# Performance work log

Hardware: AMD Instinct MI355X
Metric: run time of the kernel (lower is better)

## Reference

```python
import jax, jax.numpy as jnp
import numpy as np

BITS = 3
LEVELS = 2 ** BITS            # 8
HALF_RANGE = (LEVELS - 1) / 2  # 3.5
INCREMENT = 1.0 / (LEVELS // 2)  # 0.25


def setup_inputs() -> dict:
    key = jax.random.key(0)
    kq, kk, kv, kr = jax.random.split(key, 4)
    B, H, S, D = 2, 16, 2048, 128
    q = jax.random.normal(kq, (B, H, S, D), dtype=jnp.float32)
    k = jax.random.normal(kk, (B, H, S, D), dtype=jnp.float32)
    v = jax.random.normal(kv, (B, H, S, D), dtype=jnp.float32)
    # random orthogonal rotation (QR of a Gaussian), as in PolarQuant.__init__
    Hmat = jax.random.normal(kr, (D, D), dtype=jnp.float32)
    R, _ = jnp.linalg.qr(Hmat)
    qjl_scale = jnp.full((1,), 0.01, dtype=jnp.float32)
    return {"q": q, "k": k, "v": v, "R": R, "qjl_scale": qjl_scale}


def _compress_decompress(x, R, qjl_scale):
    """PolarQuant rotate -> QJL 3-bit quantize (+ sign correction) -> dequantize -> inverse rotate."""
    B, Hh, S, D = x.shape
    xr = jnp.einsum('bhsd,de->bhse', x, R)            # rotate: x @ R
    x_max = jnp.abs(xr).max() + 1e-8                   # global scale (as in quantize/compress)
    xs = xr / x_max * HALF_RANGE                       # scale to [-3.5, 3.5]
    xq = jnp.clip(jnp.round(xs / INCREMENT) * INCREMENT, -HALF_RANGE, HALF_RANGE)
    residual = xs - xq
    xc = xq + jnp.sign(residual) * qjl_scale[0] * x_max  # QJL 1-bit correction
    xd = xc / HALF_RANGE * x_max                       # dequantize
    xo = jnp.einsum('bhse,de->bhsd', xd, R)            # inverse rotate: y @ R.T
    return xo


def reference(q, k, v, R, qjl_scale):
    D = q.shape[-1]
    k_approx = _compress_decompress(k, R, qjl_scale)
    v_approx = _compress_decompress(v, R, qjl_scale)
    scores = jnp.einsum('bhqd,bhkd->bhqk', q, k_approx) / jnp.sqrt(jnp.float32(D))
    attn = jax.nn.softmax(scores, axis=-1)
    out = jnp.einsum('bhqk,bhkd->bhqd', attn, v_approx)
    return out
```

## Files before the change

### kernel.cpp

```cpp
#include <hip/hip_runtime.h>


typedef float    f32x4  __attribute__((ext_vector_type(4)));
typedef float    f32x16 __attribute__((ext_vector_type(16)));
typedef __bf16   bf16x8 __attribute__((ext_vector_type(8)));
typedef __bf16   bf16x4 __attribute__((ext_vector_type(4)));
typedef _Float16 f16x8  __attribute__((ext_vector_type(8)));
typedef short    s16x4  __attribute__((ext_vector_type(4)));
typedef unsigned long long u64;

#define SLEN 2048
#define DH   128

static __device__ __forceinline__ f32x16 zero16() {
  f32x16 z;
#pragma unroll
  for (int i = 0; i < 16; ++i) z[i] = 0.f;
  return z;
}

static __device__ __forceinline__ f32x16 mfma_bf16_32x32x16(bf16x8 a, bf16x8 b, f32x16 c) {
  return __builtin_amdgcn_mfma_f32_32x32x16_bf16(a, b, c, 0, 0, 0);
}
static __device__ __forceinline__ f32x16 mfma_f16_32x32x16(f16x8 a, f16x8 b, f32x16 c) {
  return __builtin_amdgcn_mfma_f32_32x32x16_f16(a, b, c, 0, 0, 0);
}
static __device__ __forceinline__ f32x16 mfma_bf16_32x32x8(s16x4 a, s16x4 b, f32x16 c) {
  return __builtin_amdgcn_mfma_f32_32x32x8bf16_1k(a, b, c, 0, 0, 0);
}

static __device__ __forceinline__ void lds_dma16(const void* g, void* l) {
  __builtin_amdgcn_global_load_lds(
      (const __attribute__((address_space(1))) void*)(unsigned long long)g,
      (__attribute__((address_space(3))) void*)(unsigned int)(unsigned long long)l,
      16, 0, 0);
}

static __device__ __forceinline__ float qdq(float xr, float xmax, float qs) {
  float xs = xr / xmax * 3.5f;
  float xq = rintf(xs * 4.0f) * 0.25f;
  xq = fminf(3.5f, fmaxf(-3.5f, xq));
  float res = xs - xq;
  float sg = (res > 0.0f) ? 1.0f : ((res < 0.0f) ? -1.0f : 0.0f);
  float xc = xq + sg * qs * xmax;
  return xc / 3.5f * xmax;
}

static __device__ __forceinline__ unsigned short bfbits(float f) {
  __bf16 b = (__bf16)f;
  return __builtin_bit_cast(unsigned short, b);
}

__global__ __launch_bounds__(256) void prep_R(
    const float* __restrict__ R, _Float16* __restrict__ Bhi,
    _Float16* __restrict__ Blo, _Float16* __restrict__ BhiT,
    _Float16* __restrict__ BloT)
{
  int i = blockIdx.x * 256 + threadIdx.x;
  int kk = i >> 7, n = i & 127;
  float r = R[i];
  _Float16 h = (_Float16)r;
  _Float16 l = (_Float16)(r - (float)h);
  Bhi[i] = h; Blo[i] = l;
  BhiT[n * 128 + kk] = h; BloT[n * 128 + kk] = l;
}

template<int NT, int MODE>
static __device__ __forceinline__ void rot_body(
    const float* __restrict__ X, const _Float16* __restrict__ Gh,
    const _Float16* __restrict__ Gl, void* __restrict__ OUTv,
    float* __restrict__ part, float* __restrict__ qn, int bid)
{
  __shared__ _Float16 BH[128 * 128];
  __shared__ _Float16 BL[(NT == 3) ? 128 * 128 : 8];

  const int tid = threadIdx.x, wave = tid >> 6, lane = tid & 63;
  const int r31 = lane & 31, hi = lane >> 5;
  const long r0 = (long)bid * 128;

#pragma unroll
  for (int u = 0; u < 8; ++u) {
    int c = (wave * 8 + u) * 64 + lane;
    int n = c >> 4, p = c & 15, ch = p ^ (n & 7);
    lds_dma16(Gh + n * 128 + ch * 8, BH + (wave * 8 + u) * 512);
    if constexpr (NT == 3)
      lds_dma16(Gl + n * 128 + ch * 8, BL + (wave * 8 + u) * 512);
  }

  const long rowg = r0 + wave * 32 + r31;
  f16x8 ah[8], al[8];
#pragma unroll
  for (int t = 0; t < 8; ++t) {
    f32x4 x0 = *(const f32x4*)&X[rowg * 128 + t * 16 + hi * 8];
    f32x4 x1 = *(const f32x4*)&X[rowg * 128 + t * 16 + hi * 8 + 4];
#pragma unroll
    for (int j = 0; j < 4; ++j) {
      _Float16 h0 = (_Float16)x0[j]; ah[t][j] = h0;
      _Float16 h1 = (_Float16)x1[j]; ah[t][4 + j] = h1;
      if constexpr (NT == 3) {
        al[t][j]     = (_Float16)(x0[j] - (float)h0);
        al[t][4 + j] = (_Float16)(x1[j] - (float)h1);
      }
    }
  }
  __syncthreads();

  f32x16 acc[4];
#pragma unroll
  for (int ct = 0; ct < 4; ++ct) acc[ct] = zero16();

#pragma unroll
  for (int ct = 0; ct < 4; ++ct) {
#pragma unroll
    for (int t = 0; t < 8; ++t) {
      int idx = (ct * 32 + r31) * 128 + (((2 * t + hi) ^ (r31 & 7)) * 8);
      f16x8 bh = *(const f16x8*)&BH[idx];
      acc[ct] = mfma_f16_32x32x16(ah[t], bh, acc[ct]);
      if constexpr (NT == 3) {
        f16x8 bl = *(const f16x8*)&BL[idx];
        acc[ct] = mfma_f16_32x32x16(ah[t], bl, acc[ct]);
        acc[ct] = mfma_f16_32x32x16(al[t], bh, acc[ct]);
      }
    }
  }

  if constexpr (MODE == 0) {
    float* OUT = (float*)OUTv;
    float am = 0.f;
#pragma unroll
    for (int ct = 0; ct < 4; ++ct)
#pragma unroll
      for (int r = 0; r < 16; ++r) {
        long grow = r0 + wave * 32 + (r & 3) + 8 * (r >> 2) + 4 * hi;
        float v = acc[ct][r];
        OUT[grow * 128 + ct * 32 + r31] = v;
        am = fmaxf(am, fabsf(v));
      }
#pragma unroll
    for (int m = 1; m <= 32; m <<= 1) am = fmaxf(am, __shfl_xor(am, m, 64));
    if (lane == 0) part[bid * 4 + wave] = am;
  } else if constexpr (MODE == 1) {
    __bf16* OUT = (__bf16*)OUTv;
    const float sc = 0.08838834764831843f;
    float rs[16];
#pragma unroll
    for (int r = 0; r < 16; ++r) rs[r] = 0.f;
#pragma unroll
    for (int ct = 0; ct < 4; ++ct)
#pragma unroll
      for (int r = 0; r < 16; ++r) {
        long grow = r0 + wave * 32 + (r & 3) + 8 * (r >> 2) + 4 * hi;
        __bf16 b = (__bf16)(acc[ct][r] * sc);
        OUT[grow * 128 + ct * 32 + r31] = b;
        float fb = (float)b;
        rs[r] += fb * fb;
      }
#pragma unroll
    for (int r = 0; r < 16; ++r) {
#pragma unroll
      for (int msk = 1; msk <= 16; msk <<= 1) rs[r] += __shfl_xor(rs[r], msk, 64);
      if (r31 == r)
        qn[r0 + wave * 32 + (r & 3) + 8 * (r >> 2) + 4 * hi] = sqrtf(rs[r]);
    }
  } else {
    float* OUT = (float*)OUTv;
#pragma unroll
    for (int ct = 0; ct < 4; ++ct)
#pragma unroll
      for (int r = 0; r < 16; ++r) {
        long grow = r0 + wave * 32 + (r & 3) + 8 * (r >> 2) + 4 * hi;
        OUT[grow * 128 + ct * 32 + r31] = acc[ct][r];
      }
  }
}

__global__ __launch_bounds__(256) void rot_kv_kernel(
    const float* __restrict__ K, const float* __restrict__ V,
    const _Float16* __restrict__ Gh, const _Float16* __restrict__ Gl,
    float* __restrict__ kr, float* __restrict__ vr,
    float* __restrict__ kpart, float* __restrict__ vpart)
{
  const bool isv = blockIdx.x >= 512;
  rot_body<3, 0>(isv ? V : K, Gh, Gl, isv ? (void*)vr : (void*)kr,
                 isv ? vpart : kpart, nullptr, blockIdx.x & 511);
}

__global__ __launch_bounds__(256) void rot_q_kernel(
    const float* __restrict__ X, const _Float16* __restrict__ Gh,
    const _Float16* __restrict__ Gl, __bf16* __restrict__ qb,
    float* __restrict__ qn)
{
  rot_body<1, 1>(X, Gh, Gl, (void*)qb, nullptr, qn, blockIdx.x);
}

__global__ __launch_bounds__(256) void rot_o_kernel(
    const float* __restrict__ X, const _Float16* __restrict__ Gh,
    const _Float16* __restrict__ Gl, float* __restrict__ out)
{
  rot_body<1, 2>(X, Gh, Gl, (void*)out, nullptr, nullptr, blockIdx.x);
}

__global__ __launch_bounds__(256) void quantize_vt_kernel(
    const float* __restrict__ vr, const float* __restrict__ vpart,
    const float* __restrict__ qjl, u64* __restrict__ vdt2)
{
  __shared__ unsigned int Ts32[128][18];
  __shared__ float sm[4];
  const int tid = threadIdx.x;

  float m = 0.f;
  for (int i = tid; i < 2048; i += 256) m = fmaxf(m, vpart[i]);
#pragma unroll
  for (int msk = 1; msk <= 32; msk <<= 1) m = fmaxf(m, __shfl_xor(m, msk, 64));
  if ((tid & 63) == 0) sm[tid >> 6] = m;
  __syncthreads();
  const float xmax = fmaxf(fmaxf(sm[0], sm[1]), fmaxf(sm[2], sm[3])) + 1e-8f;
  const float qs = qjl[0];

  const int bh = blockIdx.x >> 6, blk = blockIdx.x & 63;
  const int s0 = blk * 32;
  const int sp  = tid & 15;
  const int dch = tid >> 4;
  const long rb = (long)bh * SLEN + s0;
  const float* p0 = &vr[(rb + sp * 2    ) * 128 + dch * 8];
  const float* p1 = &vr[(rb + sp * 2 + 1) * 128 + dch * 8];
#pragma unroll
  for (int j = 0; j < 8; ++j) {
    unsigned a = bfbits(qdq(p0[j], xmax, qs));
    unsigned b = bfbits(qdq(p1[j], xmax, qs));
    Ts32[dch * 8 + j][sp] = a | (b << 16);
  }
  __syncthreads();
  const long obase = (long)(bh * 64 + blk) * 1024;
#pragma unroll
  for (int u = 0; u < 4; ++u) {
    int idx = u * 256 + tid;
    int g = idx >> 7, d = idx & 127;
    vdt2[obase + idx] = *(const u64*)&Ts32[d][2 * g];
  }
}

__global__ __launch_bounds__(256) void quantize_k_kernel(
    const float* __restrict__ kr, const float* __restrict__ kpart,
    const float* __restrict__ qjl, __bf16* __restrict__ out)
{
  __shared__ float sm[4];
  const int tid = threadIdx.x;
  float m = 0.f;
  for (int i = tid; i < 2048; i += 256) m = fmaxf(m, kpart[i]);
#pragma unroll
  for (int msk = 1; msk <= 32; msk <<= 1) m = fmaxf(m, __shfl_xor(m, msk, 64));
  if ((tid & 63) == 0) sm[tid >> 6] = m;
  __syncthreads();
  const float xmax = fmaxf(fmaxf(sm[0], sm[1]), fmaxf(sm[2], sm[3])) + 1e-8f;
  const float qs = qjl[0];

  long i = ((long)blockIdx.x * 256 + tid) * 4;
  f32x4 x = *(const f32x4*)&kr[i];
  bf16x4 ov;
#pragma unroll
  for (int j = 0; j < 4; ++j) ov[j] = (__bf16)qdq(x[j], xmax, qs);
  *(bf16x4*)&out[i] = ov;
}

__global__ __launch_bounds__(256) void attn2(
    const __bf16* __restrict__ qb, const __bf16* __restrict__ kd,
    const u64* __restrict__ vdt2, const float* __restrict__ qn,
    const float* __restrict__ kpart, const float* __restrict__ qjl,
    float* __restrict__ orot)
{
  __shared__ __attribute__((aligned(16))) __bf16 Ks[2][32 * DH];
  __shared__ __attribute__((aligned(16))) u64   Vt[2][1024];
  __shared__ float Ls[4][32];
  __shared__ float sm[4];

  const int tid = threadIdx.x, wave = tid >> 6, lane = tid & 63;
  const int r31 = lane & 31, hi = lane >> 5;
  const int head = blockIdx.x & 31, qt = blockIdx.x >> 5;
  const long hrow = (long)head * SLEN;
  const int qrow0 = qt * 128 + wave * 32;

  float km = 0.f;
  for (int i = tid; i < 2048; i += 256) km = fmaxf(km, kpart[i]);
#pragma unroll
  for (int m = 1; m <= 32; m <<= 1) km = fmaxf(km, __shfl_xor(km, m, 64));
  if (lane == 0) sm[wave] = km;
  __syncthreads();
  const float xmax = fmaxf(fmaxf(sm[0], sm[1]), fmaxf(sm[2], sm[3])) + 1e-8f;
  const float Bk = 11.313708499f * ((3.5f + qjl[0] * xmax) * xmax / 3.5f) * 1.02f * 0.5f;

  bf16x8 qf[8];
#pragma unroll
  for (int t = 0; t < 8; ++t)
    qf[t] = *(const bf16x8*)&qb[(hrow + qrow0 + r31) * DH + t * 16 + hi * 8];
  const float Mq = qn[hrow + qrow0 + r31] * Bk;

  int koff[8];
#pragma unroll
  for (int t = 0; t < 8; ++t)
    koff[t] = r31 * 256 + (((2 * t + hi) ^ (r31 & 7)) << 4);

  const __bf16* ksrc[2]; int kds[2];
#pragma unroll
  for (int u = 0; u < 2; ++u) {
    int c = (wave * 2 + u) * 64 + lane;
    int row = c >> 4, ch = (c & 15) ^ (row & 7);
    ksrc[u] = kd + (hrow + row) * DH + ch * 8;
    kds[u] = (wave * 2 + u) * 512;
  }
  const char* vbase = (const char*)(vdt2 + (long)head * 64 * 1024);
  const char* vsrc[2];
#pragma unroll
  for (int u = 0; u < 2; ++u)
    vsrc[u] = vbase + (long)((wave * 2 + u) * 64 + lane) * 16;

#pragma unroll
  for (int t0 = 0; t0 < 2; ++t0) {
    lds_dma16(ksrc[0] + (long)t0 * 32 * DH, &Ks[t0][kds[0]]);
    lds_dma16(ksrc[1] + (long)t0 * 32 * DH, &Ks[t0][kds[1]]);
    lds_dma16(vsrc[0] + (long)t0 * 8192, &Vt[t0][(wave * 2 + 0) * 128]);
    lds_dma16(vsrc[1] + (long)t0 * 8192, &Vt[t0][(wave * 2 + 1) * 128]);
  }
  asm volatile("s_waitcnt vmcnt(4)" ::: "memory");
  __builtin_amdgcn_s_barrier();
  asm volatile("" ::: "memory");

  f32x16 acc[4];
#pragma unroll
  for (int dt = 0; dt < 4; ++dt) acc[dt] = zero16();
  float ls0 = 0.f, ls1 = 0.f, ls2 = 0.f, ls3 = 0.f;

#pragma unroll 2
  for (int kt = 0; kt < SLEN / 32; ++kt) {
    const int cur = kt & 1;

    f32x16 s = zero16();
    __builtin_amdgcn_s_setprio(1);
#pragma unroll
    for (int t = 0; t < 8; ++t) {
      bf16x8 ka = *(const bf16x8*)((const char*)&Ks[cur][0] + koff[t]);
      s = mfma_bf16_32x32x16(ka, qf[t], s);
    }
    __builtin_amdgcn_s_setprio(0);

    float p[16];
#pragma unroll
    for (int r = 0; r < 16; ++r) p[r] = __expf(s[r] - Mq);
#pragma unroll
    for (int r = 0; r < 16; r += 4) {
      ls0 += p[r]; ls1 += p[r + 1]; ls2 += p[r + 2]; ls3 += p[r + 3];
    }

    __builtin_amdgcn_s_setprio(1);
#pragma unroll
    for (int st = 0; st < 4; ++st) {
      bf16x4 pb;
#pragma unroll
      for (int j = 0; j < 4; ++j) pb[j] = (__bf16)p[st * 4 + j];
      s16x4 pa = __builtin_bit_cast(s16x4, pb);
#pragma unroll
      for (int dt = 0; dt < 4; ++dt) {
        s16x4 vb = __builtin_bit_cast(s16x4, Vt[cur][(st * 2 + hi) * 128 + dt * 32 + r31]);
        acc[dt] = mfma_bf16_32x32x8(pa, vb, acc[dt]);
      }
    }
    __builtin_amdgcn_s_setprio(0);

    if (kt < SLEN / 32 - 1) {
      asm volatile("s_waitcnt vmcnt(0)" ::: "memory");
      __builtin_amdgcn_s_barrier();
      asm volatile("" ::: "memory");
      if (kt < SLEN / 32 - 2) {
        const long ko = (long)(kt + 2) * 32 * DH;
        const long vo = (long)(kt + 2) * 8192;
        lds_dma16(ksrc[0] + ko, &Ks[cur][kds[0]]);
        lds_dma16(ksrc[1] + ko, &Ks[cur][kds[1]]);
        lds_dma16(vsrc[0] + vo, &Vt[cur][(wave * 2 + 0) * 128]);
        lds_dma16(vsrc[1] + vo, &Vt[cur][(wave * 2 + 1) * 128]);
      }
    }
  }

  float lsum = (ls0 + ls1) + (ls2 + ls3);
  lsum += __shfl_xor(lsum, 32, 64);
  if (hi == 0) Ls[wave][r31] = 1.0f / lsum;
  __syncthreads();

#pragma unroll
  for (int dt = 0; dt < 4; ++dt)
#pragma unroll
    for (int r = 0; r < 16; ++r) {
      int qr = (r & 3) + 8 * (r >> 2) + 4 * hi;
      orot[(hrow + qrow0 + qr) * DH + dt * 32 + r31] = acc[dt][r] * Ls[wave][qr];
    }
}

extern "C" void kernel_launch(void* const* d_in, const int* in_sizes, int n_in,
                              void* d_out, int out_size, void* d_ws, size_t ws_size,
                              hipStream_t stream)
{
  const float* q   = (const float*)d_in[0];
  const float* k   = (const float*)d_in[1];
  const float* v   = (const float*)d_in[2];
  const float* R   = (const float*)d_in[3];
  const float* qjl = (const float*)d_in[4];

  char* ws = (char*)d_ws;
  float* kpart = (float*)ws;
  float* vpart = (float*)(ws + 8192);
  _Float16* Bhi  = (_Float16*)(ws + 32768);
  _Float16* Blo  = (_Float16*)(ws + 65536);
  _Float16* BhiT = (_Float16*)(ws + 98304);
  _Float16* BloT = (_Float16*)(ws + 131072);
  float* qn = (float*)(ws + 163840);
  char* base = ws + 425984;
  __bf16* qb   = (__bf16*)base;
  float*  kr   = (float*)(base + (16u << 20));
  float*  vr   = (float*)(base + (48u << 20));
  u64*    vdt2 = (u64*)(base + (80u << 20));
  __bf16* kd   = (__bf16*)vr;
  float* orot  = kr;

  dim3 b256(256);
  prep_R<<<64, b256, 0, stream>>>(R, Bhi, Blo, BhiT, BloT);
  rot_kv_kernel<<<1024, b256, 0, stream>>>(k, v, BhiT, BloT, kr, vr, kpart, vpart);
  rot_q_kernel<<<512, b256, 0, stream>>>(q, BhiT, BloT, qb, qn);
  quantize_vt_kernel<<<2048, b256, 0, stream>>>(vr, vpart, qjl, vdt2);
  quantize_k_kernel<<<8192, b256, 0, stream>>>(kr, kpart, qjl, kd);
  attn2<<<512, b256, 0, stream>>>(qb, kd, vdt2, qn, kpart, qjl, orot);
  rot_o_kernel<<<512, b256, 0, stream>>>(orot, Bhi, Blo, (float*)d_out);
}
```

Before: 321.3 us.

## Process two key tiles per iteration with 32x32x16 PV MFMAs and exp2 softmax

```diff
diff --git a/kernel.cpp b/kernel.cpp
--- a/kernel.cpp
+++ b/kernel.cpp
@@ -6,7 +6,6 @@
 typedef __bf16   bf16x8 __attribute__((ext_vector_type(8)));
 typedef __bf16   bf16x4 __attribute__((ext_vector_type(4)));
 typedef _Float16 f16x8  __attribute__((ext_vector_type(8)));
-typedef short    s16x4  __attribute__((ext_vector_type(4)));
 typedef unsigned long long u64;
 
 #define SLEN 2048
@@ -24,9 +23,6 @@
 }
 static __device__ __forceinline__ f32x16 mfma_f16_32x32x16(f16x8 a, f16x8 b, f32x16 c) {
   return __builtin_amdgcn_mfma_f32_32x32x16_f16(a, b, c, 0, 0, 0);
-}
-static __device__ __forceinline__ f32x16 mfma_bf16_32x32x8(s16x4 a, s16x4 b, f32x16 c) {
-  return __builtin_amdgcn_mfma_f32_32x32x8bf16_1k(a, b, c, 0, 0, 0);
 }
 
 static __device__ __forceinline__ void lds_dma16(const void* g, void* l) {
@@ -141,7 +137,7 @@
     if (lane == 0) part[bid * 4 + wave] = am;
   } else if constexpr (MODE == 1) {
     __bf16* OUT = (__bf16*)OUTv;
-    const float sc = 0.08838834764831843f;
+    const float sc = 0.12751743342f;
     float rs[16];
 #pragma unroll
     for (int r = 0; r < 16; ++r) rs[r] = 0.f;
@@ -233,10 +229,13 @@
   __syncthreads();
   const long obase = (long)(bh * 64 + blk) * 1024;
 #pragma unroll
-  for (int u = 0; u < 4; ++u) {
-    int idx = u * 256 + tid;
-    int g = idx >> 7, d = idx & 127;
-    vdt2[obase + idx] = *(const u64*)&Ts32[d][2 * g];
+  for (int uu = 0; uu < 2; ++uu) {
+    int u_ = uu * 256 + tid;
+    int half = u_ >> 8, hi = (u_ >> 7) & 1, d = u_ & 127;
+    u64 qlo = *(const u64*)&Ts32[d][2 * (half * 4 + hi)];
+    u64 qhi = *(const u64*)&Ts32[d][2 * (half * 4 + hi + 2)];
+    vdt2[obase + u_ * 2    ] = qlo;
+    vdt2[obase + u_ * 2 + 1] = qhi;
   }
 }
 
@@ -263,14 +262,14 @@
   *(bf16x4*)&out[i] = ov;
 }
 
-__global__ __launch_bounds__(256) void attn2(
+__global__ __launch_bounds__(256, 2) void attn2(
     const __bf16* __restrict__ qb, const __bf16* __restrict__ kd,
     const u64* __restrict__ vdt2, const float* __restrict__ qn,
     const float* __restrict__ kpart, const float* __restrict__ qjl,
     float* __restrict__ orot)
 {
-  __shared__ __attribute__((aligned(16))) __bf16 Ks[2][32 * DH];
-  __shared__ __attribute__((aligned(16))) u64   Vt[2][1024];
+  __shared__ __attribute__((aligned(16))) __bf16 Ks[2][2][32 * DH];
+  __shared__ __attribute__((aligned(16))) u64   Vt[2][2][1024];
   __shared__ float Ls[4][32];
   __shared__ float sm[4];
 
@@ -293,12 +292,19 @@
 #pragma unroll
   for (int t = 0; t < 8; ++t)
     qf[t] = *(const bf16x8*)&qb[(hrow + qrow0 + r31) * DH + t * 16 + hi * 8];
-  const float Mq = qn[hrow + qrow0 + r31] * Bk;
+  const float mqneg = -(qn[hrow + qrow0 + r31] * Bk);
 
   int koff[8];
 #pragma unroll
   for (int t = 0; t < 8; ++t)
     koff[t] = r31 * 256 + (((2 * t + hi) ^ (r31 & 7)) << 4);
+
+  int vof0[4], vof1[4];
+#pragma unroll
+  for (int dt = 0; dt < 4; ++dt) {
+    vof0[dt] = (((0 * 2 + hi) * 128) + dt * 32 + r31) * 16;
+    vof1[dt] = (((1 * 2 + hi) * 128) + dt * 32 + r31) * 16;
+  }
 
   const __bf16* ksrc[2]; int kds[2];
 #pragma unroll
@@ -314,14 +320,22 @@
   for (int u = 0; u < 2; ++u)
     vsrc[u] = vbase + (long)((wave * 2 + u) * 64 + lane) * 16;
 
-#pragma unroll
-  for (int t0 = 0; t0 < 2; ++t0) {
-    lds_dma16(ksrc[0] + (long)t0 * 32 * DH, &Ks[t0][kds[0]]);
-    lds_dma16(ksrc[1] + (long)t0 * 32 * DH, &Ks[t0][kds[1]]);
-    lds_dma16(vsrc[0] + (long)t0 * 8192, &Vt[t0][(wave * 2 + 0) * 128]);
-    lds_dma16(vsrc[1] + (long)t0 * 8192, &Vt[t0][(wave * 2 + 1) * 128]);
-  }
-  asm volatile("s_waitcnt vmcnt(4)" ::: "memory");
+  auto STAGE = [&](int B, int P) {
+    const long k0 = (long)(2 * P) * 32 * DH, k1 = k0 + 32 * DH;
+    const long v0 = (long)(2 * P) * 8192,    v1 = v0 + 8192;
+    lds_dma16(ksrc[0] + k0, &Ks[B][0][kds[0]]);
+    lds_dma16(ksrc[1] + k0, &Ks[B][0][kds[1]]);
+    lds_dma16(ksrc[0] + k1, &Ks[B][1][kds[0]]);
+    lds_dma16(ksrc[1] + k1, &Ks[B][1][kds[1]]);
+    lds_dma16(vsrc[0] + v0, &Vt[B][0][(wave * 2 + 0) * 128]);
+    lds_dma16(vsrc[1] + v0, &Vt[B][0][(wave * 2 + 1) * 128]);
+    lds_dma16(vsrc[0] + v1, &Vt[B][1][(wave * 2 + 0) * 128]);
+    lds_dma16(vsrc[1] + v1, &Vt[B][1][(wave * 2 + 1) * 128]);
+  };
+
+  STAGE(0, 0);
+  STAGE(1, 1);
+  asm volatile("s_waitcnt vmcnt(8)" ::: "memory");
   __builtin_amdgcn_s_barrier();
   asm volatile("" ::: "memory");
 
@@ -330,54 +344,63 @@
   for (int dt = 0; dt < 4; ++dt) acc[dt] = zero16();
   float ls0 = 0.f, ls1 = 0.f, ls2 = 0.f, ls3 = 0.f;
 
-#pragma unroll 2
-  for (int kt = 0; kt < SLEN / 32; ++kt) {
-    const int cur = kt & 1;
-
-    f32x16 s = zero16();
-    __builtin_amdgcn_s_setprio(1);
-#pragma unroll
-    for (int t = 0; t < 8; ++t) {
-      bf16x8 ka = *(const bf16x8*)((const char*)&Ks[cur][0] + koff[t]);
-      s = mfma_bf16_32x32x16(ka, qf[t], s);
-    }
-    __builtin_amdgcn_s_setprio(0);
-
+  auto TILE = [&](const f32x16& sa, const f32x16& sb, int B, int j) {
     float p[16];
 #pragma unroll
-    for (int r = 0; r < 16; ++r) p[r] = __expf(s[r] - Mq);
+    for (int r = 0; r < 16; ++r) p[r] = __builtin_amdgcn_exp2f(sa[r] + sb[r]);
 #pragma unroll
     for (int r = 0; r < 16; r += 4) {
       ls0 += p[r]; ls1 += p[r + 1]; ls2 += p[r + 2]; ls3 += p[r + 3];
     }
-
+    bf16x8 pa, pb;
+#pragma unroll
+    for (int jj = 0; jj < 8; ++jj) { pa[jj] = (__bf16)p[jj]; pb[jj] = (__bf16)p[8 + jj]; }
+    const char* vb = (const char*)&Vt[B][j][0];
     __builtin_amdgcn_s_setprio(1);
 #pragma unroll
-    for (int st = 0; st < 4; ++st) {
-      bf16x4 pb;
-#pragma unroll
-      for (int j = 0; j < 4; ++j) pb[j] = (__bf16)p[st * 4 + j];
-      s16x4 pa = __builtin_bit_cast(s16x4, pb);
-#pragma unroll
-      for (int dt = 0; dt < 4; ++dt) {
-        s16x4 vb = __builtin_bit_cast(s16x4, Vt[cur][(st * 2 + hi) * 128 + dt * 32 + r31]);
-        acc[dt] = mfma_bf16_32x32x8(pa, vb, acc[dt]);
-      }
+    for (int dt = 0; dt < 4; ++dt) {
+      bf16x8 v0 = *(const bf16x8*)(vb + vof0[dt]);
+      acc[dt] = mfma_bf16_32x32x16(pa, v0, acc[dt]);
+    }
+#pragma unroll
+    for (int dt = 0; dt < 4; ++dt) {
+      bf16x8 v1 = *(const bf16x8*)(vb + vof1[dt]);
+      acc[dt] = mfma_bf16_32x32x16(pb, v1, acc[dt]);
     }
     __builtin_amdgcn_s_setprio(0);
-
-    if (kt < SLEN / 32 - 1) {
+  };
+
+#pragma unroll 1
+  for (int i = 0; i < SLEN / 64; ++i) {
+    const int B = i & 1;
+    const char* k0 = (const char*)&Ks[B][0][0];
+    const char* k1 = (const char*)&Ks[B][1][0];
+
+    f32x16 sa0 = zero16(), sa1 = zero16(), sb0, sb1;
+#pragma unroll
+    for (int r = 0; r < 16; ++r) { sb0[r] = mqneg; sb1[r] = mqneg; }
+    __builtin_amdgcn_s_setprio(1);
+#pragma unroll
+    for (int t = 0; t < 8; t += 2) {
+      bf16x8 ka0 = *(const bf16x8*)(k0 + koff[t]);
+      bf16x8 kb0 = *(const bf16x8*)(k1 + koff[t]);
+      bf16x8 ka1 = *(const bf16x8*)(k0 + koff[t + 1]);
+      bf16x8 kb1 = *(const bf16x8*)(k1 + koff[t + 1]);
+      sa0 = mfma_bf16_32x32x16(ka0, qf[t], sa0);
+      sa1 = mfma_bf16_32x32x16(kb0, qf[t], sa1);
+      sb0 = mfma_bf16_32x32x16(ka1, qf[t + 1], sb0);
+      sb1 = mfma_bf16_32x32x16(kb1, qf[t + 1], sb1);
+    }
+    __builtin_amdgcn_s_setprio(0);
+
+    TILE(sa0, sb0, B, 0);
+    TILE(sa1, sb1, B, 1);
+
+    if (i < SLEN / 64 - 1) {
       asm volatile("s_waitcnt vmcnt(0)" ::: "memory");
       __builtin_amdgcn_s_barrier();
       asm volatile("" ::: "memory");
-      if (kt < SLEN / 32 - 2) {
-        const long ko = (long)(kt + 2) * 32 * DH;
-        const long vo = (long)(kt + 2) * 8192;
-        lds_dma16(ksrc[0] + ko, &Ks[cur][kds[0]]);
-        lds_dma16(ksrc[1] + ko, &Ks[cur][kds[1]]);
-        lds_dma16(vsrc[0] + vo, &Vt[cur][(wave * 2 + 0) * 128]);
-        lds_dma16(vsrc[1] + vo, &Vt[cur][(wave * 2 + 1) * 128]);
-      }
+      if (i < SLEN / 64 - 2) STAGE(B, i + 2);
     }
   }
 
```

New measurement: 281.4 us. 1.14x faster.

## Split attention over two key halves and combine partials in the output rotation

Applied to the files above, without the earlier changes.

```diff
diff --git a/kernel.cpp b/kernel.cpp
--- a/kernel.cpp
+++ b/kernel.cpp
@@ -6,7 +6,6 @@
 typedef __bf16   bf16x8 __attribute__((ext_vector_type(8)));
 typedef __bf16   bf16x4 __attribute__((ext_vector_type(4)));
 typedef _Float16 f16x8  __attribute__((ext_vector_type(8)));
-typedef short    s16x4  __attribute__((ext_vector_type(4)));
 typedef unsigned long long u64;
 
 #define SLEN 2048
@@ -24,9 +23,6 @@
 }
 static __device__ __forceinline__ f32x16 mfma_f16_32x32x16(f16x8 a, f16x8 b, f32x16 c) {
   return __builtin_amdgcn_mfma_f32_32x32x16_f16(a, b, c, 0, 0, 0);
-}
-static __device__ __forceinline__ f32x16 mfma_bf16_32x32x8(s16x4 a, s16x4 b, f32x16 c) {
-  return __builtin_amdgcn_mfma_f32_32x32x8bf16_1k(a, b, c, 0, 0, 0);
 }
 
 static __device__ __forceinline__ void lds_dma16(const void* g, void* l) {
@@ -141,7 +137,7 @@
     if (lane == 0) part[bid * 4 + wave] = am;
   } else if constexpr (MODE == 1) {
     __bf16* OUT = (__bf16*)OUTv;
-    const float sc = 0.08838834764831843f;
+    const float sc = 0.12751743342f;
     float rs[16];
 #pragma unroll
     for (int r = 0; r < 16; ++r) rs[r] = 0.f;
@@ -162,15 +158,6 @@
       if (r31 == r)
         qn[r0 + wave * 32 + (r & 3) + 8 * (r >> 2) + 4 * hi] = sqrtf(rs[r]);
     }
-  } else {
-    float* OUT = (float*)OUTv;
-#pragma unroll
-    for (int ct = 0; ct < 4; ++ct)
-#pragma unroll
-      for (int r = 0; r < 16; ++r) {
-        long grow = r0 + wave * 32 + (r & 3) + 8 * (r >> 2) + 4 * hi;
-        OUT[grow * 128 + ct * 32 + r31] = acc[ct][r];
-      }
   }
 }
 
@@ -193,11 +180,60 @@
   rot_body<1, 1>(X, Gh, Gl, (void*)qb, nullptr, qn, blockIdx.x);
 }
 
-__global__ __launch_bounds__(256) void rot_o_kernel(
-    const float* __restrict__ X, const _Float16* __restrict__ Gh,
-    const _Float16* __restrict__ Gl, float* __restrict__ out)
-{
-  rot_body<1, 2>(X, Gh, Gl, (void*)out, nullptr, nullptr, blockIdx.x);
+__global__ __launch_bounds__(256) void rot_oc_kernel(
+    const float* __restrict__ pA, const float* __restrict__ pB,
+    const float* __restrict__ lsumP, const _Float16* __restrict__ Gh,
+    float* __restrict__ OUT)
+{
+  __shared__ _Float16 BH[128 * 128];
+
+  const int tid = threadIdx.x, wave = tid >> 6, lane = tid & 63;
+  const int r31 = lane & 31, hi = lane >> 5;
+  const long r0 = (long)blockIdx.x * 128;
+
+#pragma unroll
+  for (int u = 0; u < 8; ++u) {
+    int c = (wave * 8 + u) * 64 + lane;
+    int n = c >> 4, p = c & 15, ch = p ^ (n & 7);
+    lds_dma16(Gh + n * 128 + ch * 8, BH + (wave * 8 + u) * 512);
+  }
+
+  const long rowg = r0 + wave * 32 + r31;
+  const float rinv = 1.0f / (lsumP[rowg] + lsumP[65536 + rowg]);
+  f16x8 ah[8];
+#pragma unroll
+  for (int t = 0; t < 8; ++t) {
+    f32x4 a0 = *(const f32x4*)&pA[rowg * 128 + t * 16 + hi * 8];
+    f32x4 a1 = *(const f32x4*)&pA[rowg * 128 + t * 16 + hi * 8 + 4];
+    f32x4 b0 = *(const f32x4*)&pB[rowg * 128 + t * 16 + hi * 8];
+    f32x4 b1 = *(const f32x4*)&pB[rowg * 128 + t * 16 + hi * 8 + 4];
+#pragma unroll
+    for (int j = 0; j < 4; ++j) {
+      ah[t][j]     = (_Float16)((a0[j] + b0[j]) * rinv);
+      ah[t][4 + j] = (_Float16)((a1[j] + b1[j]) * rinv);
+    }
+  }
+  __syncthreads();
+
+  f32x16 acc[4];
+#pragma unroll
+  for (int ct = 0; ct < 4; ++ct) acc[ct] = zero16();
+#pragma unroll
+  for (int ct = 0; ct < 4; ++ct) {
+#pragma unroll
+    for (int t = 0; t < 8; ++t) {
+      int idx = (ct * 32 + r31) * 128 + (((2 * t + hi) ^ (r31 & 7)) * 8);
+      f16x8 bh = *(const f16x8*)&BH[idx];
+      acc[ct] = mfma_f16_32x32x16(ah[t], bh, acc[ct]);
+    }
+  }
+#pragma unroll
+  for (int ct = 0; ct < 4; ++ct)
+#pragma unroll
+    for (int r = 0; r < 16; ++r) {
+      long grow = r0 + wave * 32 + (r & 3) + 8 * (r >> 2) + 4 * hi;
+      OUT[grow * 128 + ct * 32 + r31] = acc[ct][r];
+    }
 }
 
 __global__ __launch_bounds__(256) void quantize_vt_kernel(
@@ -233,10 +269,13 @@
   __syncthreads();
   const long obase = (long)(bh * 64 + blk) * 1024;
 #pragma unroll
-  for (int u = 0; u < 4; ++u) {
-    int idx = u * 256 + tid;
-    int g = idx >> 7, d = idx & 127;
-    vdt2[obase + idx] = *(const u64*)&Ts32[d][2 * g];
+  for (int uu = 0; uu < 2; ++uu) {
+    int u_ = uu * 256 + tid;
+    int half = u_ >> 8, hi = (u_ >> 7) & 1, d = u_ & 127;
+    u64 qlo = *(const u64*)&Ts32[d][2 * (half * 4 + hi)];
+    u64 qhi = *(const u64*)&Ts32[d][2 * (half * 4 + hi + 2)];
+    vdt2[obase + u_ * 2    ] = qlo;
+    vdt2[obase + u_ * 2 + 1] = qhi;
   }
 }
 
@@ -263,20 +302,22 @@
   *(bf16x4*)&out[i] = ov;
 }
 
-__global__ __launch_bounds__(256) void attn2(
+__global__ __launch_bounds__(256, 4) void attn2(
     const __bf16* __restrict__ qb, const __bf16* __restrict__ kd,
     const u64* __restrict__ vdt2, const float* __restrict__ qn,
     const float* __restrict__ kpart, const float* __restrict__ qjl,
-    float* __restrict__ orot)
+    float* __restrict__ pA, float* __restrict__ pB,
+    float* __restrict__ lsumP)
 {
   __shared__ __attribute__((aligned(16))) __bf16 Ks[2][32 * DH];
   __shared__ __attribute__((aligned(16))) u64   Vt[2][1024];
-  __shared__ float Ls[4][32];
   __shared__ float sm[4];
 
   const int tid = threadIdx.x, wave = tid >> 6, lane = tid & 63;
   const int r31 = lane & 31, hi = lane >> 5;
-  const int head = blockIdx.x & 31, qt = blockIdx.x >> 5;
+  const int bid = blockIdx.x;
+  const int kh = bid >> 9, rem = bid & 511;
+  const int head = rem & 31, qt = rem >> 5;
   const long hrow = (long)head * SLEN;
   const int qrow0 = qt * 128 + wave * 32;
 
@@ -293,37 +334,36 @@
 #pragma unroll
   for (int t = 0; t < 8; ++t)
     qf[t] = *(const bf16x8*)&qb[(hrow + qrow0 + r31) * DH + t * 16 + hi * 8];
-  const float Mq = qn[hrow + qrow0 + r31] * Bk;
+  const float mqneg = -(qn[hrow + qrow0 + r31] * Bk);
 
   int koff[8];
 #pragma unroll
   for (int t = 0; t < 8; ++t)
     koff[t] = r31 * 256 + (((2 * t + hi) ^ (r31 & 7)) << 4);
+
+  const int vbse = hi * 256 + 2 * r31;
 
   const __bf16* ksrc[2]; int kds[2];
 #pragma unroll
   for (int u = 0; u < 2; ++u) {
     int c = (wave * 2 + u) * 64 + lane;
     int row = c >> 4, ch = (c & 15) ^ (row & 7);
-    ksrc[u] = kd + (hrow + row) * DH + ch * 8;
+    ksrc[u] = kd + (hrow + kh * 1024 + row) * DH + ch * 8;
     kds[u] = (wave * 2 + u) * 512;
   }
-  const char* vbase = (const char*)(vdt2 + (long)head * 64 * 1024);
-  const char* vsrc[2];
-#pragma unroll
-  for (int u = 0; u < 2; ++u)
-    vsrc[u] = vbase + (long)((wave * 2 + u) * 64 + lane) * 16;
-
-#pragma unroll
-  for (int t0 = 0; t0 < 2; ++t0) {
-    lds_dma16(ksrc[0] + (long)t0 * 32 * DH, &Ks[t0][kds[0]]);
-    lds_dma16(ksrc[1] + (long)t0 * 32 * DH, &Ks[t0][kds[1]]);
-    lds_dma16(vsrc[0] + (long)t0 * 8192, &Vt[t0][(wave * 2 + 0) * 128]);
-    lds_dma16(vsrc[1] + (long)t0 * 8192, &Vt[t0][(wave * 2 + 1) * 128]);
-  }
-  asm volatile("s_waitcnt vmcnt(4)" ::: "memory");
-  __builtin_amdgcn_s_barrier();
-  asm volatile("" ::: "memory");
+  const char* vbase = (const char*)(vdt2 + ((long)head * 64 + kh * 32) * 1024)
+                      + (long)(wave * 2 * 64 + lane) * 16;
+
+  auto STAGE = [&](int B, int T) {
+    const long ko = (long)T * 32 * DH;
+    const long vo = (long)T * 8192;
+    lds_dma16(ksrc[0] + ko, &Ks[B][kds[0]]);
+    lds_dma16(ksrc[1] + ko, &Ks[B][kds[1]]);
+    lds_dma16(vbase + vo,        &Vt[B][(wave * 2 + 0) * 128]);
+    lds_dma16(vbase + vo + 1024, &Vt[B][(wave * 2 + 1) * 128]);
+  };
+
+  STAGE(0, 0);
 
   f32x16 acc[4];
 #pragma unroll
@@ -331,67 +371,58 @@
   float ls0 = 0.f, ls1 = 0.f, ls2 = 0.f, ls3 = 0.f;
 
 #pragma unroll 2
-  for (int kt = 0; kt < SLEN / 32; ++kt) {
-    const int cur = kt & 1;
-
-    f32x16 s = zero16();
+  for (int t = 0; t < 32; ++t) {
+    const int B = t & 1;
+    asm volatile("s_waitcnt vmcnt(0)" ::: "memory");
+    __builtin_amdgcn_s_barrier();
+    asm volatile("" ::: "memory");
+    if (t < 31) STAGE(B ^ 1, t + 1);
+
+    f32x16 s;
+#pragma unroll
+    for (int r = 0; r < 16; ++r) s[r] = mqneg;
+    const char* kb = (const char*)&Ks[B][0];
     __builtin_amdgcn_s_setprio(1);
 #pragma unroll
-    for (int t = 0; t < 8; ++t) {
-      bf16x8 ka = *(const bf16x8*)((const char*)&Ks[cur][0] + koff[t]);
-      s = mfma_bf16_32x32x16(ka, qf[t], s);
+    for (int tt = 0; tt < 8; ++tt) {
+      bf16x8 ka = *(const bf16x8*)(kb + koff[tt]);
+      s = mfma_bf16_32x32x16(ka, qf[tt], s);
     }
     __builtin_amdgcn_s_setprio(0);
 
     float p[16];
 #pragma unroll
-    for (int r = 0; r < 16; ++r) p[r] = __expf(s[r] - Mq);
+    for (int r = 0; r < 16; ++r) p[r] = __builtin_amdgcn_exp2f(s[r]);
 #pragma unroll
     for (int r = 0; r < 16; r += 4) {
       ls0 += p[r]; ls1 += p[r + 1]; ls2 += p[r + 2]; ls3 += p[r + 3];
     }
-
+    bf16x8 pa, pb;
+#pragma unroll
+    for (int jj = 0; jj < 8; ++jj) { pa[jj] = (__bf16)p[jj]; pb[jj] = (__bf16)p[8 + jj]; }
+
+    const u64* vb = &Vt[B][vbse];
     __builtin_amdgcn_s_setprio(1);
 #pragma unroll
-    for (int st = 0; st < 4; ++st) {
-      bf16x4 pb;
-#pragma unroll
-      for (int j = 0; j < 4; ++j) pb[j] = (__bf16)p[st * 4 + j];
-      s16x4 pa = __builtin_bit_cast(s16x4, pb);
-#pragma unroll
-      for (int dt = 0; dt < 4; ++dt) {
-        s16x4 vb = __builtin_bit_cast(s16x4, Vt[cur][(st * 2 + hi) * 128 + dt * 32 + r31]);
-        acc[dt] = mfma_bf16_32x32x8(pa, vb, acc[dt]);
-      }
-    }
+    for (int dt = 0; dt < 4; ++dt)
+      acc[dt] = mfma_bf16_32x32x16(pa, *(const bf16x8*)(vb + dt * 64), acc[dt]);
+#pragma unroll
+    for (int dt = 0; dt < 4; ++dt)
+      acc[dt] = mfma_bf16_32x32x16(pb, *(const bf16x8*)(vb + 512 + dt * 64), acc[dt]);
     __builtin_amdgcn_s_setprio(0);
-
-    if (kt < SLEN / 32 - 1) {
-      asm volatile("s_waitcnt vmcnt(0)" ::: "memory");
-      __builtin_amdgcn_s_barrier();
-      asm volatile("" ::: "memory");
-      if (kt < SLEN / 32 - 2) {
-        const long ko = (long)(kt + 2) * 32 * DH;
-        const long vo = (long)(kt + 2) * 8192;
-        lds_dma16(ksrc[0] + ko, &Ks[cur][kds[0]]);
-        lds_dma16(ksrc[1] + ko, &Ks[cur][kds[1]]);
-        lds_dma16(vsrc[0] + vo, &Vt[cur][(wave * 2 + 0) * 128]);
-        lds_dma16(vsrc[1] + vo, &Vt[cur][(wave * 2 + 1) * 128]);
-      }
-    }
   }
 
   float lsum = (ls0 + ls1) + (ls2 + ls3);
   lsum += __shfl_xor(lsum, 32, 64);
-  if (hi == 0) Ls[wave][r31] = 1.0f / lsum;
-  __syncthreads();
-
+  if (hi == 0) lsumP[(long)kh * 65536 + hrow + qrow0 + r31] = lsum;
+
+  float* dst = kh ? pB : pA;
 #pragma unroll
   for (int dt = 0; dt < 4; ++dt)
 #pragma unroll
     for (int r = 0; r < 16; ++r) {
       int qr = (r & 3) + 8 * (r >> 2) + 4 * hi;
-      orot[(hrow + qrow0 + qr) * DH + dt * 32 + r31] = acc[dt][r] * Ls[wave][qr];
+      dst[(hrow + qrow0 + qr) * DH + dt * 32 + r31] = acc[dt][r];
     }
 }
 
@@ -419,7 +450,9 @@
   float*  vr   = (float*)(base + (48u << 20));
   u64*    vdt2 = (u64*)(base + (80u << 20));
   __bf16* kd   = (__bf16*)vr;
+  float* lsumP = (float*)(base + (64u << 20));
   float* orot  = kr;
+  float* pB    = (float*)d_out;
 
   dim3 b256(256);
   prep_R<<<64, b256, 0, stream>>>(R, Bhi, Blo, BhiT, BloT);
@@ -427,6 +460,6 @@
   rot_q_kernel<<<512, b256, 0, stream>>>(q, BhiT, BloT, qb, qn);
   quantize_vt_kernel<<<2048, b256, 0, stream>>>(vr, vpart, qjl, vdt2);
   quantize_k_kernel<<<8192, b256, 0, stream>>>(kr, kpart, qjl, kd);
-  attn2<<<512, b256, 0, stream>>>(qb, kd, vdt2, qn, kpart, qjl, orot);
-  rot_o_kernel<<<512, b256, 0, stream>>>(orot, Bhi, Blo, (float*)d_out);
-}
+  attn2<<<1024, b256, 0, stream>>>(qb, kd, vdt2, qn, kpart, qjl, orot, pB, lsumP);
+  rot_oc_kernel<<<512, b256, 0, stream>>>(orot, pB, lsumP, Bhi, (float*)d_out);
+}
```

Measured after the change: 407.1 us. 1.27x slower.
